# Kernel optimization log

Hardware: AMD Instinct MI355X
Metric: run time of the kernel (lower is better)

## Reference

```python
import jax, jax.numpy as jnp
import numpy as np

N, E, G, D, H, C = 50000, 800000, 64, 128, 4, 32
EPS = 1e-5  # GraphNorm eps


def _gcn(x, W, b, src, dst, n):
    # PyG GCNConv: add self-loops (done by caller), symmetric norm D^-1/2 A D^-1/2
    xw = x @ W
    deg = jax.ops.segment_sum(jnp.ones_like(dst, dtype=xw.dtype), dst, num_segments=n)
    dinv = jnp.where(deg > 0, jax.lax.rsqrt(jnp.maximum(deg, 1e-12)), 0.0)
    norm = dinv[src] * dinv[dst]                      # [E2]
    out = jax.ops.segment_sum(xw[src] * norm[:, None], dst, num_segments=n)
    return out + b


def _gat(x, W, a_src, a_dst, b, src, dst, n):
    # PyG GATConv, heads=H, out C per head, concat, leaky_relu slope 0.2, self-loops added by caller
    h = (x @ W).reshape(n, H, C)
    es = jnp.einsum('nhc,hc->nh', h, a_src)
    ed = jnp.einsum('nhc,hc->nh', h, a_dst)
    e = jax.nn.leaky_relu(es[src] + ed[dst], 0.2)     # [E2,H]
    m = jax.ops.segment_max(e, dst, num_segments=n)   # per-dst softmax (stable)
    e = jnp.exp(e - m[dst])
    s = jax.ops.segment_sum(e, dst, num_segments=n)
    alpha = e / (s[dst] + 1e-16)
    out = jax.ops.segment_sum(h[src] * alpha[:, :, None], dst, num_segments=n)
    return out.reshape(n, H * C) + b


def _graphnorm(x, batch, w, b, ms, g):
    cnt = jnp.maximum(jax.ops.segment_sum(jnp.ones((x.shape[0],), x.dtype), batch, num_segments=g), 1.0)
    mean = jax.ops.segment_sum(x, batch, num_segments=g) / cnt[:, None]
    sub = x - ms * mean[batch]
    var = jax.ops.segment_sum(sub * sub, batch, num_segments=g) / cnt[:, None]
    return w * sub * jax.lax.rsqrt(var[batch] + EPS) + b


def setup_inputs() -> dict:
    key = jax.random.key(0)
    ks = jax.random.split(key, 40)

    def lin(k, din, dout):
        return jax.random.normal(k, (din, dout), jnp.float32) * np.float32((2.0 / (din + dout)) ** 0.5)

    inp = {
        'x': jax.random.normal(ks[0], (N, D), jnp.float32),
        'edge_index': jax.random.randint(ks[1], (2, E), 0, N, dtype=jnp.int32),
        'batch': jnp.sort(jax.random.randint(ks[2], (N,), 0, G, dtype=jnp.int32)),
        'Wp': lin(ks[3], D, D), 'bp': jnp.zeros((D,), jnp.float32),
        'Wg': lin(ks[4], D, D), 'bg': jnp.zeros((D,), jnp.float32),
        'Wa1': lin(ks[5], D, H * C), 'as1': jax.random.normal(ks[6], (H, C), jnp.float32) * 0.1,
        'ad1': jax.random.normal(ks[7], (H, C), jnp.float32) * 0.1, 'ba1': jnp.zeros((D,), jnp.float32),
        'Wa2': lin(ks[8], D, H * C), 'as2': jax.random.normal(ks[9], (H, C), jnp.float32) * 0.1,
        'ad2': jax.random.normal(ks[10], (H, C), jnp.float32) * 0.1, 'ba2': jnp.zeros((D,), jnp.float32),
        'gnw0': jnp.ones((D,), jnp.float32), 'gnb0': jnp.zeros((D,), jnp.float32), 'gns0': jnp.ones((D,), jnp.float32),
        'gnw1': jnp.ones((D,), jnp.float32), 'gnb1': jnp.zeros((D,), jnp.float32), 'gns1': jnp.ones((D,), jnp.float32),
        'gnw2': jnp.ones((D,), jnp.float32), 'gnb2': jnp.zeros((D,), jnp.float32), 'gns2': jnp.ones((D,), jnp.float32),
        'hw1': lin(ks[11], 2 * D, D), 'hb1': jnp.zeros((D,), jnp.float32),
        'hw2': lin(ks[12], D, D // 2), 'hb2': jnp.zeros((D // 2,), jnp.float32),
        'hw3': lin(ks[13], D // 2, 2), 'hb3': jnp.zeros((2,), jnp.float32),
        'nw1': lin(ks[14], D, D // 2), 'nb1': jnp.zeros((D // 2,), jnp.float32),
        'nw2': lin(ks[15], D // 2, 1), 'nb2': jnp.zeros((1,), jnp.float32),
    }
    return inp


def reference(x, edge_index, batch, Wp, bp, Wg, bg, Wa1, as1, ad1, ba1, Wa2, as2, ad2, ba2,
              gnw0, gnb0, gns0, gnw1, gnb1, gns1, gnw2, gnb2, gns2,
              hw1, hb1, hw2, hb2, hw3, hb3, nw1, nb1, nw2, nb2):
    n = x.shape[0]
    loop = jnp.arange(n, dtype=edge_index.dtype)
    src = jnp.concatenate([edge_index[0], loop])
    dst = jnp.concatenate([edge_index[1], loop])

    x = x @ Wp + bp
    h = _graphnorm(_gcn(x, Wg, bg, src, dst, n), batch, gnw0, gnb0, gns0, G)
    x = jax.nn.relu(h) + x  # dropout is identity in eval mode
    h = _graphnorm(_gat(x, Wa1, as1, ad1, ba1, src, dst, n), batch, gnw1, gnb1, gns1, G)
    x = jax.nn.relu(h) + x
    h = _graphnorm(_gat(x, Wa2, as2, ad2, ba2, src, dst, n), batch, gnw2, gnb2, gns2, G)
    x = jax.nn.relu(h) + x

    node_hub_scores = jax.nn.sigmoid((jax.nn.relu(x @ nw1 + nb1) @ nw2 + nb2)[:, 0])

    cnt = jnp.maximum(jax.ops.segment_sum(jnp.ones((n,), x.dtype), batch, num_segments=G), 1.0)
    gmean = jax.ops.segment_sum(x, batch, num_segments=G) / cnt[:, None]
    gmax = jax.ops.segment_max(x, batch, num_segments=G)
    graph_features = jnp.concatenate([gmean, gmax], axis=1)  # [G, 2D]

    z = jax.nn.relu(graph_features @ hw1 + hb1)
    z = jax.nn.relu(z @ hw2 + hb2)
    logits = z @ hw3 + hb3
    return (logits, node_hub_scores, graph_features, x)
```

## Files before the change

kernel.cpp:

```cpp
#include <hip/hip_runtime.h>
#include <cstdint>

#define D 128
#define GG 64
#define SLICES 16
#define NPASS 4

typedef short bf16x8 __attribute__((ext_vector_type(8)));
typedef float f32x4 __attribute__((ext_vector_type(4)));

__device__ inline unsigned short bf16u(float f) {
  unsigned u = __float_as_uint(f);
  u = (u + 0x7FFFu + ((u >> 16) & 1u)) >> 16;
  return (unsigned short)u;
}
__device__ inline float2 unpackbf2(unsigned u) {
  return make_float2(__uint_as_float(u << 16), __uint_as_float(u & 0xFFFF0000u));
}

__global__ void count_edges_k(const int* __restrict__ dst, int* __restrict__ cnt, int E) {
  int e = blockIdx.x * blockDim.x + threadIdx.x;
  if (e < E) atomicAdd(&cnt[dst[e]], 1);
}

__global__ void bounds_init_k(int* __restrict__ gstart, int* __restrict__ gend) {
  int g = threadIdx.x;
  gstart[g] = 0;
  gend[g] = 0;
}

__global__ void graph_bounds_k(const int* __restrict__ batch, int* __restrict__ gstart,
                               int* __restrict__ gend, int n) {
  int i = blockIdx.x * blockDim.x + threadIdx.x;
  if (i >= n) return;
  int b = batch[i];
  if (i == 0) {
    gstart[b] = 0;
  } else {
    int pb = batch[i - 1];
    if (pb != b) { gstart[b] = i; gend[pb] = i; }
  }
  if (i == n - 1) gend[b] = n;
}

__global__ void gcnt_k(const int* __restrict__ gstart, const int* __restrict__ gend,
                       int* __restrict__ gcnt) {
  int g = threadIdx.x;
  gcnt[g] = gend[g] - gstart[g];
}

__global__ __launch_bounds__(256) void scan1_k(const int* __restrict__ cnt, int* __restrict__ rp,
                                               int* __restrict__ bsum, int n) {
  __shared__ int sd[256];
  int t = threadIdx.x;
  int i = blockIdx.x * 256 + t;
  int v = (i < n) ? cnt[i] : 0;
  sd[t] = v;
  __syncthreads();
#pragma unroll
  for (int off = 1; off < 256; off <<= 1) {
    int u = (t >= off) ? sd[t - off] : 0;
    __syncthreads();
    sd[t] += u;
    __syncthreads();
  }
  if (i < n) rp[i] = sd[t] - v;
  if (t == 255) bsum[blockIdx.x] = sd[255];
}

__global__ __launch_bounds__(256) void scan2_k(int* __restrict__ bsum, int nb) {
  __shared__ int sd[256];
  int t = threadIdx.x;
  int v = (t < nb) ? bsum[t] : 0;
  sd[t] = v;
  __syncthreads();
#pragma unroll
  for (int off = 1; off < 256; off <<= 1) {
    int u = (t >= off) ? sd[t - off] : 0;
    __syncthreads();
    sd[t] += u;
    __syncthreads();
  }
  if (t < nb) bsum[t] = sd[t] - v;
}

__global__ __launch_bounds__(256) void scan3_k(int* __restrict__ rp, const int* __restrict__ bsum,
                                               int* __restrict__ cur, int n, int E) {
  int i = blockIdx.x * 256 + threadIdx.x;
  if (i < n) {
    int r = rp[i] + bsum[blockIdx.x];
    rp[i] = r;
    cur[i] = r;
  }
  if (i == 0) rp[n] = E;
}

__global__ __launch_bounds__(256) void fill_csr_mp_k(const int* __restrict__ src,
                                                     const int* __restrict__ dst,
                                                     int* __restrict__ cur, int* __restrict__ col,
                                                     int E, int slice, int chunks) {
  int pass = blockIdx.x / chunks;
  int e = (blockIdx.x % chunks) * 256 + threadIdx.x;
  if (e >= E) return;
  int d = dst[e];
  if (d >= pass * slice && d < (pass + 1) * slice) {
    int p = atomicAdd(&cur[d], 1);
    col[p] = src[e];
  }
}

__global__ void dinv_k(const int* __restrict__ cnt, float* __restrict__ dinv, int n) {
  int i = blockIdx.x * blockDim.x + threadIdx.x;
  if (i < n) dinv[i] = rsqrtf((float)cnt[i] + 1.0f);
}

__global__ void cast_bf16_k(const float* __restrict__ in, unsigned short* __restrict__ outp, int n4) {
  int i = blockIdx.x * blockDim.x + threadIdx.x;
  if (i >= n4) return;
  float4 v = ((const float4*)in)[i];
  ushort4 o;
  o.x = bf16u(v.x); o.y = bf16u(v.y); o.z = bf16u(v.z); o.w = bf16u(v.w);
  ((ushort4*)outp)[i] = o;
}

__global__ void packB_k(const float* __restrict__ B, unsigned short* __restrict__ Bp, int ldb, int ct) {
  int idx = blockIdx.x * 256 + threadIdx.x;
  if (idx >= ct * 256) return;
  int lane = idx & 63;
  int kc = (idx >> 6) & 3;
  int c = idx >> 8;
  int kb = kc * 32 + (lane >> 4) * 8;
  int colq = c * 16 + (lane & 15);
  unsigned short o[8];
#pragma unroll
  for (int j = 0; j < 8; ++j) o[j] = bf16u(B[(size_t)(kb + j) * ldb + colq]);
  uint4 p;
  p.x = (unsigned)o[0] | ((unsigned)o[1] << 16);
  p.y = (unsigned)o[2] | ((unsigned)o[3] << 16);
  p.z = (unsigned)o[4] | ((unsigned)o[5] << 16);
  p.w = (unsigned)o[6] | ((unsigned)o[7] << 16);
  *(uint4*)&Bp[(size_t)idx * 8] = p;
}

__global__ __launch_bounds__(256) void gemm_mfma_k(const unsigned short* __restrict__ Ab,
                                                   const unsigned short* __restrict__ Bp,
                                                   const float* __restrict__ bias,
                                                   float* __restrict__ Cf,
                                                   unsigned short* __restrict__ Cb, int M) {
  __shared__ unsigned short Bs[16384];
  int t = threadIdx.x;
  for (int i = t; i < 2048; i += 256) ((uint4*)Bs)[i] = ((const uint4*)Bp)[i];
  __syncthreads();
  int w = t >> 6, lane = t & 63;
  int row0 = blockIdx.x * 64 + w * 16;
  int arow = row0 + (lane & 15);
  f32x4 acc[8];
#pragma unroll
  for (int c = 0; c < 8; ++c) acc[c] = {0.f, 0.f, 0.f, 0.f};
#pragma unroll
  for (int kc = 0; kc < 4; ++kc) {
    bf16x8 a = {0, 0, 0, 0, 0, 0, 0, 0};
    if (arow < M) a = *(const bf16x8*)&Ab[(size_t)arow * 128 + kc * 32 + (lane >> 4) * 8];
#pragma unroll
    for (int c = 0; c < 8; ++c) {
      bf16x8 b = *(const bf16x8*)&Bs[((c * 4 + kc) * 64 + lane) * 8];
      acc[c] = __builtin_amdgcn_mfma_f32_16x16x32_bf16(a, b, acc[c], 0, 0, 0);
    }
  }
  int rbase = row0 + (lane >> 4) * 4;
#pragma unroll
  for (int c = 0; c < 8; ++c) {
    int colq = c * 16 + (lane & 15);
    float bb = bias ? bias[colq] : 0.f;
#pragma unroll
    for (int r = 0; r < 4; ++r) {
      int row = rbase + r;
      if (row < M) {
        float v = acc[c][r] + bb;
        if (Cf) Cf[(size_t)row * 128 + colq] = v;
        if (Cb) Cb[(size_t)row * 128 + colq] = bf16u(v);
      }
    }
  }
}

__global__ __launch_bounds__(256) void gcn_gather_k(const unsigned* __restrict__ xwb,
                                                    const int* __restrict__ rp, const int* __restrict__ col,
                                                    const float* __restrict__ dinv, const float* __restrict__ bias,
                                                    float* __restrict__ out, int n) {
  int i = blockIdx.x * 4 + (threadIdx.x >> 6);
  if (i >= n) return;
  int lane = threadIdx.x & 63;
  int e0 = __builtin_amdgcn_readfirstlane(rp[i]);
  int e1 = __builtin_amdgcn_readfirstlane(rp[i + 1]);
  float di = dinv[i];
  float2 sv = unpackbf2(xwb[(size_t)i * 64 + lane]);
  float ax[4], ay[4];
  ax[0] = sv.x * di * di; ay[0] = sv.y * di * di;
  ax[1] = ax[2] = ax[3] = ay[1] = ay[2] = ay[3] = 0.f;
  for (int e = e0; e < e1; e += 8) {
    int s[8]; float w[8];
#pragma unroll
    for (int j = 0; j < 8; ++j) {
      bool ok = (e + j < e1);
      s[j] = ok ? __builtin_amdgcn_readfirstlane(col[e + j]) : i;
      w[j] = ok ? dinv[s[j]] * di : 0.f;
    }
    float2 v[8];
#pragma unroll
    for (int j = 0; j < 8; ++j) v[j] = unpackbf2(xwb[(size_t)s[j] * 64 + lane]);
#pragma unroll
    for (int j = 0; j < 8; ++j) { ax[j & 3] += v[j].x * w[j]; ay[j & 3] += v[j].y * w[j]; }
  }
  float2 bb = ((const float2*)bias)[lane];
  ((float2*)out)[(size_t)i * 64 + lane] =
      make_float2(ax[0] + ax[1] + ax[2] + ax[3] + bb.x, ay[0] + ay[1] + ay[2] + ay[3] + bb.y);
}

__global__ void attn_coef_k(const unsigned short* __restrict__ hb, const float* __restrict__ a_s,
                            const float* __restrict__ a_d, float* __restrict__ es,
                            float* __restrict__ ed, int n) {
  int idx = blockIdx.x * blockDim.x + threadIdx.x;
  if (idx >= n * 4) return;
  int node = idx >> 2, hh = idx & 3;
  const uint4* hr = (const uint4*)(hb + (size_t)node * 128 + hh * 32);
  const float4* av = (const float4*)(a_s + hh * 32);
  const float4* dv = (const float4*)(a_d + hh * 32);
  float s = 0.f, d2 = 0.f;
#pragma unroll
  for (int q = 0; q < 4; ++q) {
    uint4 u = hr[q];
    float2 p0 = unpackbf2(u.x), p1 = unpackbf2(u.y), p2 = unpackbf2(u.z), p3 = unpackbf2(u.w);
    float4 a0 = av[q * 2], a1 = av[q * 2 + 1];
    float4 d0 = dv[q * 2], d1 = dv[q * 2 + 1];
    s  += p0.x * a0.x + p0.y * a0.y + p1.x * a0.z + p1.y * a0.w
        + p2.x * a1.x + p2.y * a1.y + p3.x * a1.z + p3.y * a1.w;
    d2 += p0.x * d0.x + p0.y * d0.y + p1.x * d0.z + p1.y * d0.w
        + p2.x * d1.x + p2.y * d1.y + p3.x * d1.z + p3.y * d1.w;
  }
  es[idx] = s;
  ed[idx] = d2;
}

__global__ __launch_bounds__(256) void alpha_k(const float* __restrict__ es, const float* __restrict__ ed,
                                               const int* __restrict__ rp, const int* __restrict__ col,
                                               float* __restrict__ alpha, float* __restrict__ aself,
                                               float* __restrict__ winv, int n) {
  int i = blockIdx.x * 4 + (threadIdx.x >> 6);
  if (i >= n) return;
  int lane = threadIdx.x & 63;
  int hh = lane >> 4, slot = lane & 15;
  int e0 = __builtin_amdgcn_readfirstlane(rp[i]);
  int e1 = __builtin_amdgcn_readfirstlane(rp[i + 1]);
  float edi = ed[i * 4 + hh];
  float esf = es[i * 4 + hh] + edi;
  esf = esf >= 0.f ? esf : 0.2f * esf;
  float m = esf;
  for (int e = e0 + slot; e < e1; e += 16) {
    int sj = col[e];
    float ev = es[sj * 4 + hh] + edi;
    ev = ev >= 0.f ? ev : 0.2f * ev;
    alpha[(size_t)e * 4 + hh] = ev;
    m = fmaxf(m, ev);
  }
#pragma unroll
  for (int off = 1; off < 16; off <<= 1) m = fmaxf(m, __shfl_xor(m, off, 64));
  float s = (slot == 0) ? __expf(esf - m) : 0.f;
  for (int e = e0 + slot; e < e1; e += 16) {
    float w = __expf(alpha[(size_t)e * 4 + hh] - m);
    alpha[(size_t)e * 4 + hh] = w;
    s += w;
  }
#pragma unroll
  for (int off = 1; off < 16; off <<= 1) s += __shfl_xor(s, off, 64);
  if (slot == 0) {
    aself[i * 4 + hh] = __expf(esf - m);
    winv[i * 4 + hh] = 1.0f / (s + 1e-16f);
  }
}

__global__ __launch_bounds__(256) void gat_gather_k(const unsigned* __restrict__ hfb,
                                                    const int* __restrict__ rp, const int* __restrict__ col,
                                                    const float* __restrict__ alpha, const float* __restrict__ aself,
                                                    const float* __restrict__ winv,
                                                    const float* __restrict__ bias, float* __restrict__ out, int n) {
  int i = blockIdx.x * 4 + (threadIdx.x >> 6);
  if (i >= n) return;
  int lane = threadIdx.x & 63;
  int hh = lane >> 4;
  int e0 = __builtin_amdgcn_readfirstlane(rp[i]);
  int e1 = __builtin_amdgcn_readfirstlane(rp[i + 1]);
  float2 sv = unpackbf2(hfb[(size_t)i * 64 + lane]);
  float a0 = aself[i * 4 + hh];
  float ax[4], ay[4];
  ax[0] = sv.x * a0; ay[0] = sv.y * a0;
  ax[1] = ax[2] = ax[3] = ay[1] = ay[2] = ay[3] = 0.f;
  for (int e = e0; e < e1; e += 8) {
    int s[8]; float aa[8];
#pragma unroll
    for (int j = 0; j < 8; ++j) {
      bool ok = (e + j < e1);
      s[j] = ok ? __builtin_amdgcn_readfirstlane(col[e + j]) : i;
      aa[j] = ok ? alpha[(size_t)(e + j) * 4 + hh] : 0.f;
    }
    float2 v[8];
#pragma unroll
    for (int j = 0; j < 8; ++j) v[j] = unpackbf2(hfb[(size_t)s[j] * 64 + lane]);
#pragma unroll
    for (int j = 0; j < 8; ++j) { ax[j & 3] += v[j].x * aa[j]; ay[j & 3] += v[j].y * aa[j]; }
  }
  float wi = winv[i * 4 + hh];
  float2 bb = ((const float2*)bias)[lane];
  ((float2*)out)[(size_t)i * 64 + lane] =
      make_float2((ax[0] + ax[1] + ax[2] + ax[3]) * wi + bb.x,
                  (ay[0] + ay[1] + ay[2] + ay[3]) * wi + bb.y);
}

__global__ __launch_bounds__(256) void gn_stats_k(const float* __restrict__ h, const int* __restrict__ gstart,
                                                  const int* __restrict__ gcnt, float* __restrict__ gsum,
                                                  float* __restrict__ gsq) {
  int g = blockIdx.x / SLICES, sl = blockIdx.x % SLICES;
  int st = gstart[g], cn = gcnt[g];
  int d = threadIdx.x & 127, half = threadIdx.x >> 7;
  float s = 0.f, ss = 0.f;
  for (int r = sl * 2 + half; r < cn; r += 2 * SLICES) {
    float v = h[(size_t)(st + r) * D + d];
    s += v; ss += v * v;
  }
  __shared__ float l1[128], l2[128];
  if (half) { l1[d] = s; l2[d] = ss; }
  __syncthreads();
  if (!half) {
    atomicAdd(&gsum[g * D + d], s + l1[d]);
    atomicAdd(&gsq[g * D + d], ss + l2[d]);
  }
}

__global__ void gn_finalize_k(const float* __restrict__ gsum, const float* __restrict__ gsq,
                              const int* __restrict__ gcnt, const float* __restrict__ ms,
                              float* __restrict__ mean, float* __restrict__ rstd) {
  int g = blockIdx.x, d = threadIdx.x;
  float cnt = fmaxf((float)gcnt[g], 1.0f);
  float mu = gsum[g * D + d] / cnt;
  float m2 = gsq[g * D + d] / cnt;
  float s = ms[d];
  float var = m2 - (2.0f * s - s * s) * mu * mu;
  mean[g * D + d] = mu;
  rstd[g * D + d] = rsqrtf(fmaxf(var, 0.0f) + 1e-5f);
}

__global__ void gn_apply_k(const float* __restrict__ h, float* __restrict__ x,
                           unsigned short* __restrict__ xb,
                           const int* __restrict__ batch, const float* __restrict__ mean,
                           const float* __restrict__ rstd, const float* __restrict__ w,
                           const float* __restrict__ b, const float* __restrict__ ms, int n) {
  int idx = blockIdx.x * blockDim.x + threadIdx.x;
  if (idx >= n * 32) return;
  int node = idx >> 5, q = idx & 31;
  int g = batch[node];
  int d0 = q * 4;
  float4 hv = ((const float4*)h)[idx];
  float4 xv = ((const float4*)x)[idx];
  float ha[4] = {hv.x, hv.y, hv.z, hv.w};
  float xa[4] = {xv.x, xv.y, xv.z, xv.w};
  float ra[4];
#pragma unroll
  for (int j = 0; j < 4; ++j) {
    int d = d0 + j;
    float sub = ha[j] - ms[d] * mean[g * D + d];
    float v = w[d] * sub * rstd[g * D + d] + b[d];
    ra[j] = fmaxf(v, 0.f) + xa[j];
  }
  ((float4*)x)[idx] = make_float4(ra[0], ra[1], ra[2], ra[3]);
  ushort4 o;
  o.x = bf16u(ra[0]); o.y = bf16u(ra[1]); o.z = bf16u(ra[2]); o.w = bf16u(ra[3]);
  ((ushort4*)xb)[idx] = o;
}

__global__ __launch_bounds__(256) void hub_mfma_k(const unsigned short* __restrict__ Xb,
                                                  const unsigned short* __restrict__ W1p,
                                                  const float* __restrict__ nb1, const float* __restrict__ nw2,
                                                  const float* __restrict__ nb2, float* __restrict__ out, int n) {
  __shared__ unsigned short Bs[8192];
  int t = threadIdx.x;
  for (int i = t; i < 1024; i += 256) ((uint4*)Bs)[i] = ((const uint4*)W1p)[i];
  __syncthreads();
  int w = t >> 6, lane = t & 63;
  int row0 = blockIdx.x * 64 + w * 16;
  int arow = row0 + (lane & 15);
  f32x4 acc[4];
#pragma unroll
  for (int c = 0; c < 4; ++c) acc[c] = {0.f, 0.f, 0.f, 0.f};
#pragma unroll
  for (int kc = 0; kc < 4; ++kc) {
    bf16x8 a = {0, 0, 0, 0, 0, 0, 0, 0};
    if (arow < n) a = *(const bf16x8*)&Xb[(size_t)arow * 128 + kc * 32 + (lane >> 4) * 8];
#pragma unroll
    for (int c = 0; c < 4; ++c) {
      bf16x8 b = *(const bf16x8*)&Bs[((c * 4 + kc) * 64 + lane) * 8];
      acc[c] = __builtin_amdgcn_mfma_f32_16x16x32_bf16(a, b, acc[c], 0, 0, 0);
    }
  }
  float b2 = nb2[0];
  float s[4] = {0.f, 0.f, 0.f, 0.f};
#pragma unroll
  for (int c = 0; c < 4; ++c) {
    int colq = c * 16 + (lane & 15);
    float b1 = nb1[colq];
    float w2 = nw2[colq];
#pragma unroll
    for (int r = 0; r < 4; ++r) s[r] += fmaxf(acc[c][r] + b1, 0.f) * w2;
  }
#pragma unroll
  for (int off = 1; off < 16; off <<= 1) {
#pragma unroll
    for (int r = 0; r < 4; ++r) s[r] += __shfl_xor(s[r], off, 64);
  }
  if ((lane & 15) == 0) {
    int rbase = row0 + (lane >> 4) * 4;
#pragma unroll
    for (int r = 0; r < 4; ++r) {
      int row = rbase + r;
      if (row < n) out[row] = 1.0f / (1.0f + __expf(-(s[r] + b2)));
    }
  }
}

__global__ void init_maxu_k(unsigned* __restrict__ p, int n) {
  int i = blockIdx.x * blockDim.x + threadIdx.x;
  if (i < n) p[i] = 0x007FFFFFu;
}

__global__ __launch_bounds__(256) void pool_stats_k(const float* __restrict__ x, const int* __restrict__ gstart,
                                                    const int* __restrict__ gcnt, float* __restrict__ gsum,
                                                    unsigned* __restrict__ gmaxu) {
  int g = blockIdx.x / SLICES, sl = blockIdx.x % SLICES;
  int st = gstart[g], cn = gcnt[g];
  int d = threadIdx.x & 127, half = threadIdx.x >> 7;
  float s = 0.f, mx = __uint_as_float(0xFF800000u);
  for (int r = sl * 2 + half; r < cn; r += 2 * SLICES) {
    float v = x[(size_t)(st + r) * D + d];
    s += v; mx = fmaxf(mx, v);
  }
  __shared__ float l1[128], l2[128];
  if (half) { l1[d] = s; l2[d] = mx; }
  __syncthreads();
  if (!half) {
    s += l1[d];
    mx = fmaxf(mx, l2[d]);
    atomicAdd(&gsum[g * D + d], s);
    unsigned u = __float_as_uint(mx);
    u = (u & 0x80000000u) ? ~u : (u | 0x80000000u);
    atomicMax(&gmaxu[g * D + d], u);
  }
}

__global__ void pool_fin_k(const float* __restrict__ gsum, const unsigned* __restrict__ gmaxu,
                           const int* __restrict__ gcnt, float* __restrict__ gf) {
  int g = blockIdx.x, d = threadIdx.x;
  float cnt = fmaxf((float)gcnt[g], 1.0f);
  gf[g * 256 + d] = gsum[g * D + d] / cnt;
  unsigned u = gmaxu[g * D + d];
  unsigned bits = (u & 0x80000000u) ? (u ^ 0x80000000u) : ~u;
  gf[g * 256 + 128 + d] = __uint_as_float(bits);
}

__global__ __launch_bounds__(128) void mlp_k(const float* __restrict__ gf, const float* __restrict__ hw1,
                                             const float* __restrict__ hb1, const float* __restrict__ hw2,
                                             const float* __restrict__ hb2, const float* __restrict__ hw3,
                                             const float* __restrict__ hb3, float* __restrict__ logits) {
  __shared__ float sg[256], z1[128], z2[64];
  int g = blockIdx.x, t = threadIdx.x;
  sg[t] = gf[g * 256 + t];
  sg[t + 128] = gf[g * 256 + 128 + t];
  __syncthreads();
  float a = hb1[t];
  for (int k = 0; k < 256; ++k) a += sg[k] * hw1[k * 128 + t];
  z1[t] = fmaxf(a, 0.f);
  __syncthreads();
  if (t < 64) {
    float a2 = hb2[t];
    for (int k = 0; k < 128; ++k) a2 += z1[k] * hw2[k * 64 + t];
    z2[t] = fmaxf(a2, 0.f);
  }
  __syncthreads();
  if (t < 2) {
    float a3 = hb3[t];
    for (int k = 0; k < 64; ++k) a3 += z2[k] * hw3[k * 2 + t];
    logits[g * 2 + t] = a3;
  }
}

extern "C" void kernel_launch(void* const* d_in, const int* in_sizes, int n_in,
                              void* d_out, int out_size, void* d_ws, size_t ws_size,
                              hipStream_t stream) {
  const float* x_in  = (const float*)d_in[0];
  const int*   eidx  = (const int*)d_in[1];
  const int*   batch = (const int*)d_in[2];
  const float* Wp  = (const float*)d_in[3];
  const float* bp  = (const float*)d_in[4];
  const float* Wg  = (const float*)d_in[5];
  const float* bg  = (const float*)d_in[6];
  const float* Wa1 = (const float*)d_in[7];
  const float* as1 = (const float*)d_in[8];
  const float* ad1 = (const float*)d_in[9];
  const float* ba1 = (const float*)d_in[10];
  const float* Wa2 = (const float*)d_in[11];
  const float* as2 = (const float*)d_in[12];
  const float* ad2 = (const float*)d_in[13];
  const float* ba2 = (const float*)d_in[14];
  const float* gnw[3] = {(const float*)d_in[15], (const float*)d_in[18], (const float*)d_in[21]};
  const float* gnb[3] = {(const float*)d_in[16], (const float*)d_in[19], (const float*)d_in[22]};
  const float* gns[3] = {(const float*)d_in[17], (const float*)d_in[20], (const float*)d_in[23]};
  const float* hw1 = (const float*)d_in[24];
  const float* hb1 = (const float*)d_in[25];
  const float* hw2 = (const float*)d_in[26];
  const float* hb2 = (const float*)d_in[27];
  const float* hw3 = (const float*)d_in[28];
  const float* hb3 = (const float*)d_in[29];
  const float* nw1 = (const float*)d_in[30];
  const float* nb1 = (const float*)d_in[31];
  const float* nw2 = (const float*)d_in[32];
  const float* nb2 = (const float*)d_in[33];

  const int N = in_sizes[0] / D;
  const int E = in_sizes[1] / 2;
  const int* src = eidx;
  const int* dst = eidx + E;

  float* out    = (float*)d_out;
  float* logits = out;
  float* hub    = out + GG * 2;
  float* gf     = out + GG * 2 + N;
  float* X      = out + GG * 2 + N + GG * 256;

  char* wp = (char*)d_ws;
  auto alloc = [&](size_t bytes) { char* p = wp; wp += (bytes + 255) & ~(size_t)255; return p; };
  float*    B1    = (float*)alloc((size_t)N * D * 4);
  float*    B2    = (float*)alloc((size_t)N * D * 4);
  unsigned* B1h   = (unsigned*)alloc((size_t)N * (D / 2) * 4);
  unsigned short* Xb = (unsigned short*)alloc((size_t)N * D * 2);
  int*   col     = (int*)alloc((size_t)E * 4);
  int*   cnt     = (int*)alloc((size_t)N * 4);
  int*   rowp    = (int*)alloc((size_t)(N + 1) * 4);
  int*   cur     = (int*)alloc((size_t)N * 4);
  float* dinv    = (float*)alloc((size_t)N * 4);
  float* es      = (float*)alloc((size_t)N * 4 * 4);
  float* ed      = (float*)alloc((size_t)N * 4 * 4);
  float* aself   = (float*)alloc((size_t)N * 4 * 4);
  float* winv    = (float*)alloc((size_t)N * 4 * 4);
  float* gsum    = (float*)alloc((size_t)GG * D * 4);
  float* gsq     = (float*)alloc((size_t)GG * D * 4);
  unsigned* gmaxu = (unsigned*)alloc((size_t)GG * D * 4);
  float* mean    = (float*)alloc((size_t)GG * D * 4);
  float* rstd    = (float*)alloc((size_t)GG * D * 4);
  int*   gcnt    = (int*)alloc((size_t)GG * 4);
  int*   gstart  = (int*)alloc((size_t)GG * 4);
  int*   gend    = (int*)alloc((size_t)GG * 4);
  int*   bsum    = (int*)alloc((size_t)256 * 4);
  unsigned short* Wpp  = (unsigned short*)alloc(16384 * 2);
  unsigned short* Wgp  = (unsigned short*)alloc(16384 * 2);
  unsigned short* Wa1p = (unsigned short*)alloc(16384 * 2);
  unsigned short* Wa2p = (unsigned short*)alloc(16384 * 2);
  unsigned short* W1p  = (unsigned short*)alloc(8192 * 2);
  float* alpha = B1;
  unsigned short* xinb = (unsigned short*)B2;
  if ((size_t)(wp - (char*)d_ws) > ws_size) return;

  const int nb = (N + 255) / 256;

  hipMemsetAsync(cnt, 0, (size_t)N * 4, stream);
  count_edges_k<<<(E + 255) / 256, 256, 0, stream>>>(dst, cnt, E);
  bounds_init_k<<<1, GG, 0, stream>>>(gstart, gend);
  graph_bounds_k<<<nb, 256, 0, stream>>>(batch, gstart, gend, N);
  gcnt_k<<<1, GG, 0, stream>>>(gstart, gend, gcnt);
  scan1_k<<<nb, 256, 0, stream>>>(cnt, rowp, bsum, N);
  scan2_k<<<1, 256, 0, stream>>>(bsum, nb);
  scan3_k<<<nb, 256, 0, stream>>>(rowp, bsum, cur, N, E);
  dinv_k<<<nb, 256, 0, stream>>>(cnt, dinv, N);
  {
    int chunks = (E + 255) / 256;
    int slice = (N + NPASS - 1) / NPASS;
    fill_csr_mp_k<<<chunks * NPASS, 256, 0, stream>>>(src, dst, cur, col, E, slice, chunks);
  }

  packB_k<<<8, 256, 0, stream>>>(Wp, Wpp, 128, 8);
  packB_k<<<8, 256, 0, stream>>>(Wg, Wgp, 128, 8);
  packB_k<<<8, 256, 0, stream>>>(Wa1, Wa1p, 128, 8);
  packB_k<<<8, 256, 0, stream>>>(Wa2, Wa2p, 128, 8);
  packB_k<<<4, 256, 0, stream>>>(nw1, W1p, 64, 4);
  cast_bf16_k<<<(N * 32 + 255) / 256, 256, 0, stream>>>(x_in, xinb, N * 32);

  const int gemmGrid = (N + 63) / 64;
  const int aggGrid  = (N + 3) / 4;

  auto graphnorm = [&](int layer) {
    hipMemsetAsync(gsum, 0, 2 * (size_t)GG * D * 4, stream);
    gn_stats_k<<<GG * SLICES, 256, 0, stream>>>(B2, gstart, gcnt, gsum, gsq);
    gn_finalize_k<<<GG, D, 0, stream>>>(gsum, gsq, gcnt, gns[layer], mean, rstd);
    gn_apply_k<<<(N * 32 + 255) / 256, 256, 0, stream>>>(B2, X, Xb, batch, mean, rstd,
                                                         gnw[layer], gnb[layer], gns[layer], N);
  };

  gemm_mfma_k<<<gemmGrid, 256, 0, stream>>>(xinb, Wpp, bp, X, Xb, N);

  gemm_mfma_k<<<gemmGrid, 256, 0, stream>>>(Xb, Wgp, nullptr, nullptr, (unsigned short*)B1h, N);
  gcn_gather_k<<<aggGrid, 256, 0, stream>>>(B1h, rowp, col, dinv, bg, B2, N);
  graphnorm(0);

  gemm_mfma_k<<<gemmGrid, 256, 0, stream>>>(Xb, Wa1p, nullptr, nullptr, (unsigned short*)B1h, N);
  attn_coef_k<<<(N * 4 + 255) / 256, 256, 0, stream>>>((const unsigned short*)B1h, as1, ad1, es, ed, N);
  alpha_k<<<aggGrid, 256, 0, stream>>>(es, ed, rowp, col, alpha, aself, winv, N);
  gat_gather_k<<<aggGrid, 256, 0, stream>>>(B1h, rowp, col, alpha, aself, winv, ba1, B2, N);
  graphnorm(1);

  gemm_mfma_k<<<gemmGrid, 256, 0, stream>>>(Xb, Wa2p, nullptr, nullptr, (unsigned short*)B1h, N);
  attn_coef_k<<<(N * 4 + 255) / 256, 256, 0, stream>>>((const unsigned short*)B1h, as2, ad2, es, ed, N);
  alpha_k<<<aggGrid, 256, 0, stream>>>(es, ed, rowp, col, alpha, aself, winv, N);
  gat_gather_k<<<aggGrid, 256, 0, stream>>>(B1h, rowp, col, alpha, aself, winv, ba2, B2, N);
  graphnorm(2);

  hub_mfma_k<<<gemmGrid, 256, 0, stream>>>(Xb, W1p, nb1, nw2, nb2, hub, N);

  hipMemsetAsync(gsum, 0, (size_t)GG * D * 4, stream);
  init_maxu_k<<<(GG * D + 255) / 256, 256, 0, stream>>>(gmaxu, GG * D);
  pool_stats_k<<<GG * SLICES, 256, 0, stream>>>(X, gstart, gcnt, gsum, gmaxu);
  pool_fin_k<<<GG, D, 0, stream>>>(gsum, gmaxu, gcnt, gf);
  mlp_k<<<GG, 128, 0, stream>>>(gf, hw1, hb1, hw2, hb2, hw3, hb3, logits);
}
```

Before: 471.3 us.

## Split wavefront into four 16-lane groups gathering different edges with 16-byte loads

The GCN and GAT gather kernels now split each 64-lane wavefront into four 16-lane groups. Each group fetches a whole 256-byte bf16 row with uint4 loads, and the four groups work on different neighbor edges at once. The per-group partial sums are combined with cross-lane shuffles, and one group writes the output with float4 stores. The aim is more memory-level parallelism and wider loads on the irregular gather, at the cost of per-lane (non-uniform) index loads and an extra shuffle reduction.

```diff
diff --git a/kernel.cpp b/kernel.cpp
--- a/kernel.cpp
+++ b/kernel.cpp
@@ -16,6 +16,11 @@
 }
 __device__ inline float2 unpackbf2(unsigned u) {
   return make_float2(__uint_as_float(u << 16), __uint_as_float(u & 0xFFFF0000u));
+}
+__device__ inline void accum8(float* acc, uint4 v, float w) {
+  float2 p0 = unpackbf2(v.x), p1 = unpackbf2(v.y), p2 = unpackbf2(v.z), p3 = unpackbf2(v.w);
+  acc[0] += p0.x * w; acc[1] += p0.y * w; acc[2] += p1.x * w; acc[3] += p1.y * w;
+  acc[4] += p2.x * w; acc[5] += p2.y * w; acc[6] += p3.x * w; acc[7] += p3.y * w;
 }
 
 __global__ void count_edges_k(const int* __restrict__ dst, int* __restrict__ cnt, int E) {
@@ -184,37 +189,54 @@
   }
 }
 
-__global__ __launch_bounds__(256) void gcn_gather_k(const unsigned* __restrict__ xwb,
+__global__ __launch_bounds__(256) void gcn_gather_k(const uint4* __restrict__ xw16,
                                                     const int* __restrict__ rp, const int* __restrict__ col,
                                                     const float* __restrict__ dinv, const float* __restrict__ bias,
                                                     float* __restrict__ out, int n) {
   int i = blockIdx.x * 4 + (threadIdx.x >> 6);
   if (i >= n) return;
   int lane = threadIdx.x & 63;
+  int g = lane >> 4, sub = lane & 15;
   int e0 = __builtin_amdgcn_readfirstlane(rp[i]);
   int e1 = __builtin_amdgcn_readfirstlane(rp[i + 1]);
   float di = dinv[i];
-  float2 sv = unpackbf2(xwb[(size_t)i * 64 + lane]);
-  float ax[4], ay[4];
-  ax[0] = sv.x * di * di; ay[0] = sv.y * di * di;
-  ax[1] = ax[2] = ax[3] = ay[1] = ay[2] = ay[3] = 0.f;
-  for (int e = e0; e < e1; e += 8) {
-    int s[8]; float w[8];
-#pragma unroll
-    for (int j = 0; j < 8; ++j) {
-      bool ok = (e + j < e1);
-      s[j] = ok ? __builtin_amdgcn_readfirstlane(col[e + j]) : i;
-      w[j] = ok ? dinv[s[j]] * di : 0.f;
-    }
-    float2 v[8];
-#pragma unroll
-    for (int j = 0; j < 8; ++j) v[j] = unpackbf2(xwb[(size_t)s[j] * 64 + lane]);
-#pragma unroll
-    for (int j = 0; j < 8; ++j) { ax[j & 3] += v[j].x * w[j]; ay[j & 3] += v[j].y * w[j]; }
-  }
-  float2 bb = ((const float2*)bias)[lane];
-  ((float2*)out)[(size_t)i * 64 + lane] =
-      make_float2(ax[0] + ax[1] + ax[2] + ax[3] + bb.x, ay[0] + ay[1] + ay[2] + ay[3] + bb.y);
+  float acc[8] = {0.f, 0.f, 0.f, 0.f, 0.f, 0.f, 0.f, 0.f};
+  if (g == 0) {
+    uint4 v = xw16[(size_t)i * 16 + sub];
+    accum8(acc, v, di * di);
+  }
+  int e = e0;
+  for (; e + 15 < e1; e += 16) {
+    int s0 = col[e + g];
+    int s1 = col[e + 4 + g];
+    int s2 = col[e + 8 + g];
+    int s3 = col[e + 12 + g];
+    float w0 = dinv[s0] * di, w1 = dinv[s1] * di, w2 = dinv[s2] * di, w3 = dinv[s3] * di;
+    uint4 v0 = xw16[(size_t)s0 * 16 + sub];
+    uint4 v1 = xw16[(size_t)s1 * 16 + sub];
+    uint4 v2 = xw16[(size_t)s2 * 16 + sub];
+    uint4 v3 = xw16[(size_t)s3 * 16 + sub];
+    accum8(acc, v0, w0); accum8(acc, v1, w1); accum8(acc, v2, w2); accum8(acc, v3, w3);
+  }
+  for (; e < e1; e += 4) {
+    bool ok = (e + g) < e1;
+    int s0 = ok ? col[e + g] : i;
+    float w0 = ok ? dinv[s0] * di : 0.f;
+    uint4 v0 = xw16[(size_t)s0 * 16 + sub];
+    accum8(acc, v0, w0);
+  }
+#pragma unroll
+  for (int k = 0; k < 8; ++k) {
+    acc[k] += __shfl_xor(acc[k], 16, 64);
+    acc[k] += __shfl_xor(acc[k], 32, 64);
+  }
+  if (g == 0) {
+    float4 b0 = ((const float4*)bias)[sub * 2], b1 = ((const float4*)bias)[sub * 2 + 1];
+    *(float4*)&out[(size_t)i * 128 + sub * 8] =
+        make_float4(acc[0] + b0.x, acc[1] + b0.y, acc[2] + b0.z, acc[3] + b0.w);
+    *(float4*)&out[(size_t)i * 128 + sub * 8 + 4] =
+        make_float4(acc[4] + b1.x, acc[5] + b1.y, acc[6] + b1.z, acc[7] + b1.w);
+  }
 }
 
 __global__ void attn_coef_k(const unsigned short* __restrict__ hb, const float* __restrict__ a_s,
@@ -279,7 +301,7 @@
   }
 }
 
-__global__ __launch_bounds__(256) void gat_gather_k(const unsigned* __restrict__ hfb,
+__global__ __launch_bounds__(256) void gat_gather_k(const uint4* __restrict__ hf16,
                                                     const int* __restrict__ rp, const int* __restrict__ col,
                                                     const float* __restrict__ alpha, const float* __restrict__ aself,
                                                     const float* __restrict__ winv,
@@ -287,33 +309,51 @@
   int i = blockIdx.x * 4 + (threadIdx.x >> 6);
   if (i >= n) return;
   int lane = threadIdx.x & 63;
-  int hh = lane >> 4;
+  int g = lane >> 4, sub = lane & 15;
+  int hh = sub >> 2;
   int e0 = __builtin_amdgcn_readfirstlane(rp[i]);
   int e1 = __builtin_amdgcn_readfirstlane(rp[i + 1]);
-  float2 sv = unpackbf2(hfb[(size_t)i * 64 + lane]);
-  float a0 = aself[i * 4 + hh];
-  float ax[4], ay[4];
-  ax[0] = sv.x * a0; ay[0] = sv.y * a0;
-  ax[1] = ax[2] = ax[3] = ay[1] = ay[2] = ay[3] = 0.f;
-  for (int e = e0; e < e1; e += 8) {
-    int s[8]; float aa[8];
-#pragma unroll
-    for (int j = 0; j < 8; ++j) {
-      bool ok = (e + j < e1);
-      s[j] = ok ? __builtin_amdgcn_readfirstlane(col[e + j]) : i;
-      aa[j] = ok ? alpha[(size_t)(e + j) * 4 + hh] : 0.f;
-    }
-    float2 v[8];
-#pragma unroll
-    for (int j = 0; j < 8; ++j) v[j] = unpackbf2(hfb[(size_t)s[j] * 64 + lane]);
-#pragma unroll
-    for (int j = 0; j < 8; ++j) { ax[j & 3] += v[j].x * aa[j]; ay[j & 3] += v[j].y * aa[j]; }
-  }
-  float wi = winv[i * 4 + hh];
-  float2 bb = ((const float2*)bias)[lane];
-  ((float2*)out)[(size_t)i * 64 + lane] =
-      make_float2((ax[0] + ax[1] + ax[2] + ax[3]) * wi + bb.x,
-                  (ay[0] + ay[1] + ay[2] + ay[3]) * wi + bb.y);
+  float acc[8] = {0.f, 0.f, 0.f, 0.f, 0.f, 0.f, 0.f, 0.f};
+  if (g == 0) {
+    uint4 v = hf16[(size_t)i * 16 + sub];
+    accum8(acc, v, aself[i * 4 + hh]);
+  }
+  int e = e0;
+  for (; e + 15 < e1; e += 16) {
+    int s0 = col[e + g];
+    int s1 = col[e + 4 + g];
+    int s2 = col[e + 8 + g];
+    int s3 = col[e + 12 + g];
+    float a0 = alpha[(size_t)(e + g) * 4 + hh];
+    float a1 = alpha[(size_t)(e + 4 + g) * 4 + hh];
+    float a2 = alpha[(size_t)(e + 8 + g) * 4 + hh];
+    float a3 = alpha[(size_t)(e + 12 + g) * 4 + hh];
+    uint4 v0 = hf16[(size_t)s0 * 16 + sub];
+    uint4 v1 = hf16[(size_t)s1 * 16 + sub];
+    uint4 v2 = hf16[(size_t)s2 * 16 + sub];
+    uint4 v3 = hf16[(size_t)s3 * 16 + sub];
+    accum8(acc, v0, a0); accum8(acc, v1, a1); accum8(acc, v2, a2); accum8(acc, v3, a3);
+  }
+  for (; e < e1; e += 4) {
+    bool ok = (e + g) < e1;
+    int s0 = ok ? col[e + g] : i;
+    float a0 = ok ? alpha[(size_t)(e + g) * 4 + hh] : 0.f;
+    uint4 v0 = hf16[(size_t)s0 * 16 + sub];
+    accum8(acc, v0, a0);
+  }
+#pragma unroll
+  for (int k = 0; k < 8; ++k) {
+    acc[k] += __shfl_xor(acc[k], 16, 64);
+    acc[k] += __shfl_xor(acc[k], 32, 64);
+  }
+  if (g == 0) {
+    float wi = winv[i * 4 + hh];
+    float4 b0 = ((const float4*)bias)[sub * 2], b1 = ((const float4*)bias)[sub * 2 + 1];
+    *(float4*)&out[(size_t)i * 128 + sub * 8] =
+        make_float4(acc[0] * wi + b0.x, acc[1] * wi + b0.y, acc[2] * wi + b0.z, acc[3] * wi + b0.w);
+    *(float4*)&out[(size_t)i * 128 + sub * 8 + 4] =
+        make_float4(acc[4] * wi + b1.x, acc[5] * wi + b1.y, acc[6] * wi + b1.z, acc[7] * wi + b1.w);
+  }
 }
 
 __global__ __launch_bounds__(256) void gn_stats_k(const float* __restrict__ h, const int* __restrict__ gstart,
@@ -605,19 +645,19 @@
   gemm_mfma_k<<<gemmGrid, 256, 0, stream>>>(xinb, Wpp, bp, X, Xb, N);
 
   gemm_mfma_k<<<gemmGrid, 256, 0, stream>>>(Xb, Wgp, nullptr, nullptr, (unsigned short*)B1h, N);
-  gcn_gather_k<<<aggGrid, 256, 0, stream>>>(B1h, rowp, col, dinv, bg, B2, N);
+  gcn_gather_k<<<aggGrid, 256, 0, stream>>>((const uint4*)B1h, rowp, col, dinv, bg, B2, N);
   graphnorm(0);
 
   gemm_mfma_k<<<gemmGrid, 256, 0, stream>>>(Xb, Wa1p, nullptr, nullptr, (unsigned short*)B1h, N);
   attn_coef_k<<<(N * 4 + 255) / 256, 256, 0, stream>>>((const unsigned short*)B1h, as1, ad1, es, ed, N);
   alpha_k<<<aggGrid, 256, 0, stream>>>(es, ed, rowp, col, alpha, aself, winv, N);
-  gat_gather_k<<<aggGrid, 256, 0, stream>>>(B1h, rowp, col, alpha, aself, winv, ba1, B2, N);
+  gat_gather_k<<<aggGrid, 256, 0, stream>>>((const uint4*)B1h, rowp, col, alpha, aself, winv, ba1, B2, N);
   graphnorm(1);
 
   gemm_mfma_k<<<gemmGrid, 256, 0, stream>>>(Xb, Wa2p, nullptr, nullptr, (unsigned short*)B1h, N);
   attn_coef_k<<<(N * 4 + 255) / 256, 256, 0, stream>>>((const unsigned short*)B1h, as2, ad2, es, ed, N);
   alpha_k<<<aggGrid, 256, 0, stream>>>(es, ed, rowp, col, alpha, aself, winv, N);
-  gat_gather_k<<<aggGrid, 256, 0, stream>>>(B1h, rowp, col, alpha, aself, winv, ba2, B2, N);
+  gat_gather_k<<<aggGrid, 256, 0, stream>>>((const uint4*)B1h, rowp, col, alpha, aself, winv, ba2, B2, N);
   graphnorm(2);
 
   hub_mfma_k<<<gemmGrid, 256, 0, stream>>>(Xb, W1p, nb1, nw2, nb2, hub, N);
```

Result: faster. 458.2 us (-2.8%).
